# Optimization experiments

Hardware: AMD Instinct MI355X
Metric: run time of the kernel (lower is better)

## Reference

```python
import jax, jax.numpy as jnp
import numpy as np

B, N, NINP, NFEAT, H = 4096, 4096, 64, 32, 4


def setup_inputs() -> dict:
    key = jax.random.key(0)
    ks = jax.random.split(key, 8)
    s_in = 1.0 / np.sqrt(NINP)
    s_att = 1.0 / np.sqrt(2 * NFEAT)
    return {
        "X": jax.random.normal(ks[0], (B, NINP), jnp.float32),
        "G": jax.random.normal(ks[1], (N, NINP), jnp.float32),
        "A": jax.random.uniform(ks[2], (B, N), jnp.float32),  # additive mask
        "W": jax.random.uniform(ks[3], (H, NINP, NFEAT), jnp.float32, -s_in, s_in),
        "b": jax.random.uniform(ks[4], (H, NFEAT), jnp.float32, -s_in, s_in),
        "a_src": jax.random.uniform(ks[5], (H, NFEAT), jnp.float32, -s_att, s_att),
        "a_dst": jax.random.uniform(ks[6], (H, NFEAT), jnp.float32, -s_att, s_att),
        "att_b": jax.random.uniform(ks[7], (H,), jnp.float32, -s_att, s_att),
    }


def reference(X, G, A, W, b, a_src, a_dst, att_b):
    # Per-head linear transforms (all heads batched via einsum)
    WX = jnp.einsum("bi,hif->bhf", X, W) + b            # (B, H, F)
    WG = jnp.einsum("ni,hif->nhf", G, W) + b            # (N, H, F)
    # Decomposed concat-attention: a^T [WX_b ; WG_n] = a_src.WX_b + a_dst.WG_n
    s_src = jnp.einsum("bhf,hf->bh", WX, a_src)         # (B, H)
    s_dst = jnp.einsum("nhf,hf->nh", WG, a_dst)         # (N, H)
    e = s_src[:, :, None] + s_dst.T[None, :, :] + att_b[None, :, None]  # (B,H,N)
    att = jax.nn.softmax(e - A[:, None, :], axis=-1)    # adjacency-masked softmax
    # Dropout(0.5) is identity in eval mode (deterministic reference).
    out = jnp.einsum("bhn,nhf->bhf", att, WG)           # weighted aggregation
    out = jax.nn.relu(out)                              # activation before concat
    return out.reshape(out.shape[0], -1)                # (B, H*F) concat heads
```

## Files before the change

### kernel.cpp

```cpp
#include <hip/hip_runtime.h>
#include <stdint.h>

#define N_TOK 4096
#define D_IN  64
#define NF    32
#define NH    4
#define OUTW  (NH * NF)
#define NT    8
#define CHUNK 128
#define BT    32

typedef float        f32x4  __attribute__((ext_vector_type(4)));
typedef unsigned int uint4v __attribute__((ext_vector_type(4)));
typedef __bf16       bf16x8 __attribute__((ext_vector_type(8)));

union Frag { uint4v u; bf16x8 v; };

static __device__ __forceinline__ unsigned short f2bf_rne(float x) {
  unsigned u = __float_as_uint(x);
  u += 0x7fffu + ((u >> 16) & 1u);
  return (unsigned short)(u >> 16);
}

__global__ __launch_bounds__(128) void prep_kernel(
    const float* __restrict__ G, const float* __restrict__ W,
    const float* __restrict__ bias, const float* __restrict__ a_dst,
    unsigned short* __restrict__ PB) {
  __shared__ float gs[NT * D_IN];
  const int tid = threadIdx.x;
  const int n0  = blockIdx.x * NT;
  {
    const float4* src = (const float4*)(G + (size_t)n0 * D_IN);
    float4* dst = (float4*)gs;
    dst[tid] = src[tid];
  }
  __syncthreads();
  const int h = tid >> 5, f = tid & 31;
  float acc[NT];
  const float bb = bias[h * NF + f];
#pragma unroll
  for (int k = 0; k < NT; ++k) acc[k] = bb;
#pragma unroll
  for (int i = 0; i < D_IN; ++i) {
    const float wv = W[(h * D_IN + i) * NF + f];
#pragma unroll
    for (int k = 0; k < NT; ++k) acc[k] = fmaf(gs[k * D_IN + i], wv, acc[k]);
  }
  const float ad = a_dst[h * NF + f];
  float ev[NT];
#pragma unroll
  for (int k = 0; k < NT; ++k) {
    float s = acc[k] * ad;
    s += __shfl_xor(s, 1);  s += __shfl_xor(s, 2);  s += __shfl_xor(s, 4);
    s += __shfl_xor(s, 8);  s += __shfl_xor(s, 16);
    ev[k] = __expf(s);
  }
  const int t   = n0 >> 5;
  const int gq  = (n0 >> 3) & 3;
  const int set = (h << 1) | (f >> 4);
  const int col = f & 15;
  union { uint4 u4; unsigned short us[8]; } pk;
#pragma unroll
  for (int k = 0; k < NT; ++k) pk.us[k] = f2bf_rne(acc[k] * ev[k]);
  *(uint4*)(PB + (size_t)((((t * 9 + set) << 6) + (gq << 4) + col)) * 8) = pk.u4;
  if (f == 0) {
    union { uint4 u4; unsigned short us[8]; } pe;
#pragma unroll
    for (int k = 0; k < NT; ++k) pe.us[k] = f2bf_rne(ev[k]);
    *(uint4*)(PB + (size_t)((((t * 9 + 8) << 6) + (gq << 4) + h)) * 8) = pe.u4;
  }
  if (h == 0 && f >= 4 && f < 16) {
    uint4 z; z.x = 0u; z.y = 0u; z.z = 0u; z.w = 0u;
    *(uint4*)(PB + (size_t)((((t * 9 + 8) << 6) + (gq << 4) + f)) * 8) = z;
  }
}

template <int NS>
__global__ __launch_bounds__(512) void attn_kernel(
    const float* __restrict__ A, const unsigned short* __restrict__ PB,
    float* __restrict__ op, float* __restrict__ dp, float* __restrict__ out) {
  constexpr int NHALF  = N_TOK / NS;
  constexpr int NIT    = NHALF / CHUNK;
  constexpr int RINGSZ = BT * CHUNK * 2;
  __shared__ __align__(16) unsigned short ring[3 * BT * CHUNK];
  __shared__ float denLds[BT * NH];
  char* ringb = (char*)ring;

  const int tid  = threadIdx.x;
  const int lane = tid & 63;
  const int w    = tid >> 6;
  const int bid  = blockIdx.x;
  const int s    = bid & (NS - 1);
  const int b0   = (bid / NS) * BT;

  const int srow = tid >> 4, tp = tid & 15;
  const float* abase = A + (size_t)(b0 + srow) * N_TOK + s * NHALF + tp * 8;
  const int wb0 = srow * 256 + ((tp ^ (srow & 15)) << 4);

  const int rowm = lane & 15, g = lane >> 4;
  const char* pbb  = (const char*)PB + (size_t)s * (NHALF / 32) * 9216;
  const char* pown = pbb + (((w << 6) + lane) << 4);
  const char* pden = pbb + (((8 << 6) + lane) << 4);

  f32x4 acc0  = {0.f, 0.f, 0.f, 0.f}, acc1  = {0.f, 0.f, 0.f, 0.f};
  f32x4 accd0 = {0.f, 0.f, 0.f, 0.f}, accd1 = {0.f, 0.f, 0.f, 0.f};
  f32x4 aXa, aXb, aYa, aYb;
  Frag bo0, bo1, bo2, bo3, bd0, bd1, bd2, bd3;
  Frag co0, co1, co2, co3, cd0, cd1, cd2, cd3;
  int mR = 0, mW = 1;

#define LOADA2(d0, d1, cc) do {                                                \
    const float* ap_ = abase + (size_t)(cc) * CHUNK;                           \
    asm volatile("global_load_dwordx4 %0, %1, off"                            \
                 : "=v"(d0) : "v"(ap_) : "memory");                            \
    asm volatile("global_load_dwordx4 %0, %1, off"                            \
                 : "=v"(d1) : "v"(ap_ + 4) : "memory");                        \
  } while (0)
#define LOADBO(fr, cc, kk)                                                     \
  asm volatile("global_load_dwordx4 %0, %1, off"                              \
               : "=v"(fr.u)                                                    \
               : "v"(pown + (size_t)((cc) * 4 + (kk)) * 9216) : "memory")
#define LOADBD(fr, cc, kk)                                                     \
  asm volatile("global_load_dwordx4 %0, %1, off"                              \
               : "=v"(fr.u)                                                    \
               : "v"(pden + (size_t)((cc) * 4 + (kk)) * 9216) : "memory")

#define EXPP(AV0, AV1, mw) do {                                                \
    float x0 = __expf(-AV0[0]), x1 = __expf(-AV0[1]);                          \
    float x2 = __expf(-AV0[2]), x3 = __expf(-AV0[3]);                          \
    float x4 = __expf(-AV1[0]), x5 = __expf(-AV1[1]);                          \
    float x6 = __expf(-AV1[2]), x7 = __expf(-AV1[3]);                          \
    uint4v t_;                                                                 \
    t_[0] = __builtin_amdgcn_perm(__float_as_uint(x1), __float_as_uint(x0), 0x07060302u); \
    t_[1] = __builtin_amdgcn_perm(__float_as_uint(x3), __float_as_uint(x2), 0x07060302u); \
    t_[2] = __builtin_amdgcn_perm(__float_as_uint(x5), __float_as_uint(x4), 0x07060302u); \
    t_[3] = __builtin_amdgcn_perm(__float_as_uint(x7), __float_as_uint(x6), 0x07060302u); \
    *(uint4v*)(ringb + (mw) * RINGSZ + wb0) = t_;                              \
  } while (0)

#define MSTEPD(rg, kk, FB, FD) do {                                            \
    Frag af_;                                                                  \
    af_.v = *(const bf16x8*)(ringb + mR * RINGSZ + ((rg) * 16 + rowm) * 256 +  \
                             ((((kk) * 4 + g) ^ rowm) << 4));                  \
    if ((rg) == 0) {                                                           \
      acc0  = __builtin_amdgcn_mfma_f32_16x16x32_bf16(af_.v, FB.v, acc0,  0, 0, 0); \
      accd0 = __builtin_amdgcn_mfma_f32_16x16x32_bf16(af_.v, FD.v, accd0, 0, 0, 0); \
    } else {                                                                   \
      acc1  = __builtin_amdgcn_mfma_f32_16x16x32_bf16(af_.v, FB.v, acc1,  0, 0, 0); \
      accd1 = __builtin_amdgcn_mfma_f32_16x16x32_bf16(af_.v, FD.v, accd1, 0, 0, 0); \
    }                                                                          \
  } while (0)
#define MSTEPO(rg, kk, FB) do {                                                \
    Frag af_;                                                                  \
    af_.v = *(const bf16x8*)(ringb + mR * RINGSZ + ((rg) * 16 + rowm) * 256 +  \
                             ((((kk) * 4 + g) ^ rowm) << 4));                  \
    if ((rg) == 0)                                                             \
      acc0 = __builtin_amdgcn_mfma_f32_16x16x32_bf16(af_.v, FB.v, acc0, 0, 0, 0); \
    else                                                                       \
      acc1 = __builtin_amdgcn_mfma_f32_16x16x32_bf16(af_.v, FB.v, acc1, 0, 0, 0); \
  } while (0)

#define ITERD(cc, AC0, AC1, AN0, AN1, CO0, CO1, CO2, CO3, CD0, CD1, CD2, CD3,  \
              NO0, NO1, NO2, NO3, ND0, ND1, ND2, ND3) do {                     \
    { const int cb_ = ((cc) + 1 < NIT) ? (cc) + 1 : NIT - 1;                   \
      LOADBO(NO0, cb_, 0); LOADBO(NO1, cb_, 1);                                \
      LOADBO(NO2, cb_, 2); LOADBO(NO3, cb_, 3);                                \
      LOADBD(ND0, cb_, 0); LOADBD(ND1, cb_, 1);                                \
      LOADBD(ND2, cb_, 2); LOADBD(ND3, cb_, 3); }                              \
    { const int ca_ = ((cc) + 2 < NIT) ? (cc) + 2 : NIT - 1;                   \
      LOADA2(AN0, AN1, ca_); }                                                 \
    asm volatile("s_waitcnt vmcnt(10)" ::: "memory");                          \
    __builtin_amdgcn_sched_barrier(0);                                         \
    EXPP(AC0, AC1, mW);                                                        \
    asm volatile("s_waitcnt lgkmcnt(0)" ::: "memory");                         \
    __builtin_amdgcn_sched_barrier(0);                                         \
    __builtin_amdgcn_s_barrier();                                              \
    MSTEPD(0, 0, CO0, CD0); MSTEPD(1, 0, CO0, CD0);                            \
    MSTEPD(0, 1, CO1, CD1); MSTEPD(1, 1, CO1, CD1);                            \
    MSTEPD(0, 2, CO2, CD2); MSTEPD(1, 2, CO2, CD2);                            \
    MSTEPD(0, 3, CO3, CD3); MSTEPD(1, 3, CO3, CD3);                            \
    mR = mW; mW = (mW + 1 == 3) ? 0 : mW + 1;                                  \
  } while (0)
#define ITERO(cc, AC0, AC1, AN0, AN1, CO0, CO1, CO2, CO3,                      \
              NO0, NO1, NO2, NO3) do {                                         \
    { const int cb_ = ((cc) + 1 < NIT) ? (cc) + 1 : NIT - 1;                   \
      LOADBO(NO0, cb_, 0); LOADBO(NO1, cb_, 1);                                \
      LOADBO(NO2, cb_, 2); LOADBO(NO3, cb_, 3); }                              \
    { const int ca_ = ((cc) + 2 < NIT) ? (cc) + 2 : NIT - 1;                   \
      LOADA2(AN0, AN1, ca_); }                                                 \
    asm volatile("s_waitcnt vmcnt(6)" ::: "memory");                           \
    __builtin_amdgcn_sched_barrier(0);                                         \
    EXPP(AC0, AC1, mW);                                                        \
    asm volatile("s_waitcnt lgkmcnt(0)" ::: "memory");                         \
    __builtin_amdgcn_sched_barrier(0);                                         \
    __builtin_amdgcn_s_barrier();                                              \
    MSTEPO(0, 0, CO0); MSTEPO(1, 0, CO0);                                      \
    MSTEPO(0, 1, CO1); MSTEPO(1, 1, CO1);                                      \
    MSTEPO(0, 2, CO2); MSTEPO(1, 2, CO2);                                      \
    MSTEPO(0, 3, CO3); MSTEPO(1, 3, CO3);                                      \
    mR = mW; mW = (mW + 1 == 3) ? 0 : mW + 1;                                  \
  } while (0)

  if (w == 0) {
    LOADA2(aXa, aXb, 0);
    LOADBO(bo0, 0, 0); LOADBO(bo1, 0, 1); LOADBO(bo2, 0, 2); LOADBO(bo3, 0, 3);
    LOADBD(bd0, 0, 0); LOADBD(bd1, 0, 1); LOADBD(bd2, 0, 2); LOADBD(bd3, 0, 3);
    LOADA2(aYa, aYb, 1);
    asm volatile("s_waitcnt vmcnt(10)" ::: "memory");
    __builtin_amdgcn_sched_barrier(0);
    EXPP(aXa, aXb, 0);
#pragma unroll 1
    for (int i = 0; i < NIT; i += 2) {
      ITERD(i,     aYa, aYb, aXa, aXb, bo0, bo1, bo2, bo3, bd0, bd1, bd2, bd3,
                                       co0, co1, co2, co3, cd0, cd1, cd2, cd3);
      ITERD(i + 1, aXa, aXb, aYa, aYb, co0, co1, co2, co3, cd0, cd1, cd2, cd3,
                                       bo0, bo1, bo2, bo3, bd0, bd1, bd2, bd3);
    }
  } else {
    LOADA2(aXa, aXb, 0);
    LOADBO(bo0, 0, 0); LOADBO(bo1, 0, 1); LOADBO(bo2, 0, 2); LOADBO(bo3, 0, 3);
    LOADA2(aYa, aYb, 1);
    asm volatile("s_waitcnt vmcnt(6)" ::: "memory");
    __builtin_amdgcn_sched_barrier(0);
    EXPP(aXa, aXb, 0);
#pragma unroll 1
    for (int i = 0; i < NIT; i += 2) {
      ITERO(i,     aYa, aYb, aXa, aXb, bo0, bo1, bo2, bo3,
                                       co0, co1, co2, co3);
      ITERO(i + 1, aXa, aXb, aYa, aYb, co0, co1, co2, co3,
                                       bo0, bo1, bo2, bo3);
    }
  }

  asm volatile("s_waitcnt vmcnt(0)" ::: "memory");
  __builtin_amdgcn_sched_barrier(0);

  if (NS == 1) {
    if (w == 0 && rowm < NH) {
#pragma unroll
      for (int r = 0; r < 4; ++r) {
        denLds[(g * 4 + r) * NH + rowm]      = accd0[r];
        denLds[(16 + g * 4 + r) * NH + rowm] = accd1[r];
      }
    }
    __syncthreads();
    const int hh = w >> 1;
#pragma unroll
    for (int r = 0; r < 4; ++r) {
      const float o0 = acc0[r] / denLds[(g * 4 + r) * NH + hh];
      out[(size_t)(b0 + g * 4 + r) * OUTW + w * 16 + rowm] = o0 > 0.f ? o0 : 0.f;
      const float o1 = acc1[r] / denLds[(16 + g * 4 + r) * NH + hh];
      out[(size_t)(b0 + 16 + g * 4 + r) * OUTW + w * 16 + rowm] = o1 > 0.f ? o1 : 0.f;
    }
  } else {
    float* ob = op + (size_t)s * (N_TOK * OUTW) + (size_t)b0 * OUTW + w * 16 + rowm;
#pragma unroll
    for (int r = 0; r < 4; ++r) {
      ob[(size_t)(g * 4 + r) * OUTW]      = acc0[r];
      ob[(size_t)(16 + g * 4 + r) * OUTW] = acc1[r];
    }
    if (w == 0 && rowm < NH) {
#pragma unroll
      for (int r = 0; r < 4; ++r) {
        dp[((size_t)s * N_TOK + b0 + g * 4 + r) * NH + rowm]      = accd0[r];
        dp[((size_t)s * N_TOK + b0 + 16 + g * 4 + r) * NH + rowm] = accd1[r];
      }
    }
  }
#undef LOADA2
#undef LOADBO
#undef LOADBD
#undef EXPP
#undef MSTEPD
#undef MSTEPO
#undef ITERD
#undef ITERO
}

__global__ __launch_bounds__(256) void comb_kernel(
    const float* __restrict__ op, const float* __restrict__ dp,
    float* __restrict__ out, int NS) {
  const int idx4 = blockIdx.x * 256 + threadIdx.x;
  const int eb = idx4 >> 5;
  const int h  = ((idx4 << 2) & 127) >> 5;
  float4 o; o.x = 0.f; o.y = 0.f; o.z = 0.f; o.w = 0.f;
  float d = 0.f;
  for (int s2 = 0; s2 < NS; ++s2) {
    float4 vv = *(const float4*)(op + (size_t)s2 * (N_TOK * OUTW) + (size_t)idx4 * 4);
    o.x += vv.x; o.y += vv.y; o.z += vv.z; o.w += vv.w;
    d += dp[((size_t)s2 * N_TOK + eb) * NH + h];
  }
  const float r = 1.f / d;
  float4 res;
  res.x = fmaxf(o.x * r, 0.f);
  res.y = fmaxf(o.y * r, 0.f);
  res.z = fmaxf(o.z * r, 0.f);
  res.w = fmaxf(o.w * r, 0.f);
  *(float4*)(out + (size_t)idx4 * 4) = res;
}

extern "C" void kernel_launch(void* const* d_in, const int* in_sizes, int n_in,
                              void* d_out, int out_size, void* d_ws, size_t ws_size,
                              hipStream_t stream) {
  const float* G     = (const float*)d_in[1];
  const float* A     = (const float*)d_in[2];
  const float* W     = (const float*)d_in[3];
  const float* bias  = (const float*)d_in[4];
  const float* a_dst = (const float*)d_in[6];

  char* ws = (char*)d_ws;
  const size_t PBsz = (size_t)128 * 9 * 1024;
  const size_t per_split = (size_t)N_TOK * OUTW * 4 + (size_t)N_TOK * NH * 4;

  unsigned short* PB = (unsigned short*)ws;
  float* op = (float*)(ws + PBsz);
  float* outp = (float*)d_out;

  prep_kernel<<<N_TOK / NT, 128, 0, stream>>>(G, W, bias, a_dst, PB);
  if (ws_size >= PBsz + 4 * per_split) {
    float* dp = (float*)(ws + PBsz + 4 * (size_t)N_TOK * OUTW * 4);
    attn_kernel<4><<<(N_TOK / BT) * 4, 512, 0, stream>>>(A, PB, op, dp, nullptr);
    comb_kernel<<<(N_TOK * OUTW / 4) / 256, 256, 0, stream>>>(op, dp, outp, 4);
  } else if (ws_size >= PBsz + 2 * per_split) {
    float* dp = (float*)(ws + PBsz + 2 * (size_t)N_TOK * OUTW * 4);
    attn_kernel<2><<<(N_TOK / BT) * 2, 512, 0, stream>>>(A, PB, op, dp, nullptr);
    comb_kernel<<<(N_TOK * OUTW / 4) / 256, 256, 0, stream>>>(op, dp, outp, 2);
  } else {
    attn_kernel<1><<<N_TOK / BT, 512, 0, stream>>>(A, PB, nullptr, nullptr, outp);
  }
}
```

Measured before the change: 30.83 us.

## Double batch tile to 64 rows per block to reuse B fragments

Raises the batch tile per attention block from 32 to 64 rows. Each wave now keeps four accumulator groups and issues 16 MFMAs per chunk against the same loaded PB fragments, so per-row global loads of the projected G data are halved. Each thread now loads and exponentiates 16 mask values per chunk instead of 8. The cost is more register pressure, a larger LDS ring, and half as many blocks, which can hurt occupancy and how well the GPU is filled.

```diff
diff --git a/kernel.cpp b/kernel.cpp
--- a/kernel.cpp
+++ b/kernel.cpp
@@ -8,7 +8,7 @@
 #define OUTW  (NH * NF)
 #define NT    8
 #define CHUNK 128
-#define BT    32
+#define BT    64
 
 typedef float        f32x4  __attribute__((ext_vector_type(4)));
 typedef unsigned int uint4v __attribute__((ext_vector_type(4)));
@@ -93,9 +93,10 @@
   const int s    = bid & (NS - 1);
   const int b0   = (bid / NS) * BT;
 
-  const int srow = tid >> 4, tp = tid & 15;
-  const float* abase = A + (size_t)(b0 + srow) * N_TOK + s * NHALF + tp * 8;
-  const int wb0 = srow * 256 + ((tp ^ (srow & 15)) << 4);
+  const int srow = tid >> 3, tp = tid & 7;
+  const float* abase = A + (size_t)(b0 + srow) * N_TOK + s * NHALF + tp * 16;
+  const int wb0 = srow * 256 + (((tp * 2    ) ^ (srow & 15)) << 4);
+  const int wb1 = srow * 256 + (((tp * 2 + 1) ^ (srow & 15)) << 4);
 
   const int rowm = lane & 15, g = lane >> 4;
   const char* pbb  = (const char*)PB + (size_t)s * (NHALF / 32) * 9216;
@@ -103,18 +104,24 @@
   const char* pden = pbb + (((8 << 6) + lane) << 4);
 
   f32x4 acc0  = {0.f, 0.f, 0.f, 0.f}, acc1  = {0.f, 0.f, 0.f, 0.f};
+  f32x4 acc2  = {0.f, 0.f, 0.f, 0.f}, acc3  = {0.f, 0.f, 0.f, 0.f};
   f32x4 accd0 = {0.f, 0.f, 0.f, 0.f}, accd1 = {0.f, 0.f, 0.f, 0.f};
-  f32x4 aXa, aXb, aYa, aYb;
+  f32x4 accd2 = {0.f, 0.f, 0.f, 0.f}, accd3 = {0.f, 0.f, 0.f, 0.f};
+  f32x4 aXa, aXb, aXc, aXd, aYa, aYb, aYc, aYd;
   Frag bo0, bo1, bo2, bo3, bd0, bd1, bd2, bd3;
   Frag co0, co1, co2, co3, cd0, cd1, cd2, cd3;
   int mR = 0, mW = 1;
 
-#define LOADA2(d0, d1, cc) do {                                                \
+#define LOADA4(d0, d1, d2, d3, cc) do {                                        \
     const float* ap_ = abase + (size_t)(cc) * CHUNK;                           \
     asm volatile("global_load_dwordx4 %0, %1, off"                            \
                  : "=v"(d0) : "v"(ap_) : "memory");                            \
     asm volatile("global_load_dwordx4 %0, %1, off"                            \
                  : "=v"(d1) : "v"(ap_ + 4) : "memory");                        \
+    asm volatile("global_load_dwordx4 %0, %1, off"                            \
+                 : "=v"(d2) : "v"(ap_ + 8) : "memory");                        \
+    asm volatile("global_load_dwordx4 %0, %1, off"                            \
+                 : "=v"(d3) : "v"(ap_ + 12) : "memory");                       \
   } while (0)
 #define LOADBO(fr, cc, kk)                                                     \
   asm volatile("global_load_dwordx4 %0, %1, off"                              \
@@ -125,42 +132,44 @@
                : "=v"(fr.u)                                                    \
                : "v"(pden + (size_t)((cc) * 4 + (kk)) * 9216) : "memory")
 
-#define EXPP(AV0, AV1, mw) do {                                                \
+#define EXPP(AV0, AV1, AV2, AV3, mw) do {                                      \
     float x0 = __expf(-AV0[0]), x1 = __expf(-AV0[1]);                          \
     float x2 = __expf(-AV0[2]), x3 = __expf(-AV0[3]);                          \
     float x4 = __expf(-AV1[0]), x5 = __expf(-AV1[1]);                          \
     float x6 = __expf(-AV1[2]), x7 = __expf(-AV1[3]);                          \
-    uint4v t_;                                                                 \
+    float y0 = __expf(-AV2[0]), y1 = __expf(-AV2[1]);                          \
+    float y2 = __expf(-AV2[2]), y3 = __expf(-AV2[3]);                          \
+    float y4 = __expf(-AV3[0]), y5 = __expf(-AV3[1]);                          \
+    float y6 = __expf(-AV3[2]), y7 = __expf(-AV3[3]);                          \
+    uint4v t_, u_;                                                             \
     t_[0] = __builtin_amdgcn_perm(__float_as_uint(x1), __float_as_uint(x0), 0x07060302u); \
     t_[1] = __builtin_amdgcn_perm(__float_as_uint(x3), __float_as_uint(x2), 0x07060302u); \
     t_[2] = __builtin_amdgcn_perm(__float_as_uint(x5), __float_as_uint(x4), 0x07060302u); \
     t_[3] = __builtin_amdgcn_perm(__float_as_uint(x7), __float_as_uint(x6), 0x07060302u); \
-    *(uint4v*)(ringb + (mw) * RINGSZ + wb0) = t_;                              \
-  } while (0)
-
-#define MSTEPD(rg, kk, FB, FD) do {                                            \
-    Frag af_;                                                                  \
-    af_.v = *(const bf16x8*)(ringb + mR * RINGSZ + ((rg) * 16 + rowm) * 256 +  \
-                             ((((kk) * 4 + g) ^ rowm) << 4));                  \
-    if ((rg) == 0) {                                                           \
-      acc0  = __builtin_amdgcn_mfma_f32_16x16x32_bf16(af_.v, FB.v, acc0,  0, 0, 0); \
-      accd0 = __builtin_amdgcn_mfma_f32_16x16x32_bf16(af_.v, FD.v, accd0, 0, 0, 0); \
-    } else {                                                                   \
-      acc1  = __builtin_amdgcn_mfma_f32_16x16x32_bf16(af_.v, FB.v, acc1,  0, 0, 0); \
-      accd1 = __builtin_amdgcn_mfma_f32_16x16x32_bf16(af_.v, FD.v, accd1, 0, 0, 0); \
-    }                                                                          \
-  } while (0)
-#define MSTEPO(rg, kk, FB) do {                                                \
-    Frag af_;                                                                  \
-    af_.v = *(const bf16x8*)(ringb + mR * RINGSZ + ((rg) * 16 + rowm) * 256 +  \
-                             ((((kk) * 4 + g) ^ rowm) << 4));                  \
-    if ((rg) == 0)                                                             \
-      acc0 = __builtin_amdgcn_mfma_f32_16x16x32_bf16(af_.v, FB.v, acc0, 0, 0, 0); \
-    else                                                                       \
-      acc1 = __builtin_amdgcn_mfma_f32_16x16x32_bf16(af_.v, FB.v, acc1, 0, 0, 0); \
-  } while (0)
-
-#define ITERD(cc, AC0, AC1, AN0, AN1, CO0, CO1, CO2, CO3, CD0, CD1, CD2, CD3,  \
+    u_[0] = __builtin_amdgcn_perm(__float_as_uint(y1), __float_as_uint(y0), 0x07060302u); \
+    u_[1] = __builtin_amdgcn_perm(__float_as_uint(y3), __float_as_uint(y2), 0x07060302u); \
+    u_[2] = __builtin_amdgcn_perm(__float_as_uint(y5), __float_as_uint(y4), 0x07060302u); \
+    u_[3] = __builtin_amdgcn_perm(__float_as_uint(y7), __float_as_uint(y6), 0x07060302u); \
+    char* rb_ = ringb + (mw) * RINGSZ;                                         \
+    *(uint4v*)(rb_ + wb0) = t_;                                                \
+    *(uint4v*)(rb_ + wb1) = u_;                                                \
+  } while (0)
+
+#define AF(rg, kk)                                                             \
+  (*(const bf16x8*)(ringb + mR * RINGSZ + ((rg) * 16 + rowm) * 256 +           \
+                    ((((kk) * 4 + g) ^ rowm) << 4)))
+#define MQD(ACC, ACCD, rg, kk, FB, FD) do {                                    \
+    Frag af_; af_.v = AF(rg, kk);                                              \
+    ACC  = __builtin_amdgcn_mfma_f32_16x16x32_bf16(af_.v, FB.v, ACC,  0, 0, 0);\
+    ACCD = __builtin_amdgcn_mfma_f32_16x16x32_bf16(af_.v, FD.v, ACCD, 0, 0, 0);\
+  } while (0)
+#define MQO(ACC, rg, kk, FB) do {                                              \
+    Frag af_; af_.v = AF(rg, kk);                                              \
+    ACC = __builtin_amdgcn_mfma_f32_16x16x32_bf16(af_.v, FB.v, ACC, 0, 0, 0);  \
+  } while (0)
+
+#define ITERD(cc, AC0, AC1, AC2, AC3, AN0, AN1, AN2, AN3,                      \
+              CO0, CO1, CO2, CO3, CD0, CD1, CD2, CD3,                          \
               NO0, NO1, NO2, NO3, ND0, ND1, ND2, ND3) do {                     \
     { const int cb_ = ((cc) + 1 < NIT) ? (cc) + 1 : NIT - 1;                   \
       LOADBO(NO0, cb_, 0); LOADBO(NO1, cb_, 1);                                \
@@ -168,67 +177,77 @@
       LOADBD(ND0, cb_, 0); LOADBD(ND1, cb_, 1);                                \
       LOADBD(ND2, cb_, 2); LOADBD(ND3, cb_, 3); }                              \
     { const int ca_ = ((cc) + 2 < NIT) ? (cc) + 2 : NIT - 1;                   \
-      LOADA2(AN0, AN1, ca_); }                                                 \
-    asm volatile("s_waitcnt vmcnt(10)" ::: "memory");                          \
+      LOADA4(AN0, AN1, AN2, AN3, ca_); }                                       \
+    asm volatile("s_waitcnt vmcnt(12)" ::: "memory");                          \
     __builtin_amdgcn_sched_barrier(0);                                         \
-    EXPP(AC0, AC1, mW);                                                        \
+    EXPP(AC0, AC1, AC2, AC3, mW);                                              \
     asm volatile("s_waitcnt lgkmcnt(0)" ::: "memory");                         \
     __builtin_amdgcn_sched_barrier(0);                                         \
     __builtin_amdgcn_s_barrier();                                              \
-    MSTEPD(0, 0, CO0, CD0); MSTEPD(1, 0, CO0, CD0);                            \
-    MSTEPD(0, 1, CO1, CD1); MSTEPD(1, 1, CO1, CD1);                            \
-    MSTEPD(0, 2, CO2, CD2); MSTEPD(1, 2, CO2, CD2);                            \
-    MSTEPD(0, 3, CO3, CD3); MSTEPD(1, 3, CO3, CD3);                            \
+    MQD(acc0, accd0, 0, 0, CO0, CD0); MQD(acc1, accd1, 1, 0, CO0, CD0);        \
+    MQD(acc2, accd2, 2, 0, CO0, CD0); MQD(acc3, accd3, 3, 0, CO0, CD0);        \
+    MQD(acc0, accd0, 0, 1, CO1, CD1); MQD(acc1, accd1, 1, 1, CO1, CD1);        \
+    MQD(acc2, accd2, 2, 1, CO1, CD1); MQD(acc3, accd3, 3, 1, CO1, CD1);        \
+    MQD(acc0, accd0, 0, 2, CO2, CD2); MQD(acc1, accd1, 1, 2, CO2, CD2);        \
+    MQD(acc2, accd2, 2, 2, CO2, CD2); MQD(acc3, accd3, 3, 2, CO2, CD2);        \
+    MQD(acc0, accd0, 0, 3, CO3, CD3); MQD(acc1, accd1, 1, 3, CO3, CD3);        \
+    MQD(acc2, accd2, 2, 3, CO3, CD3); MQD(acc3, accd3, 3, 3, CO3, CD3);        \
     mR = mW; mW = (mW + 1 == 3) ? 0 : mW + 1;                                  \
   } while (0)
-#define ITERO(cc, AC0, AC1, AN0, AN1, CO0, CO1, CO2, CO3,                      \
-              NO0, NO1, NO2, NO3) do {                                         \
+#define ITERO(cc, AC0, AC1, AC2, AC3, AN0, AN1, AN2, AN3,                      \
+              CO0, CO1, CO2, CO3, NO0, NO1, NO2, NO3) do {                     \
     { const int cb_ = ((cc) + 1 < NIT) ? (cc) + 1 : NIT - 1;                   \
       LOADBO(NO0, cb_, 0); LOADBO(NO1, cb_, 1);                                \
       LOADBO(NO2, cb_, 2); LOADBO(NO3, cb_, 3); }                              \
     { const int ca_ = ((cc) + 2 < NIT) ? (cc) + 2 : NIT - 1;                   \
-      LOADA2(AN0, AN1, ca_); }                                                 \
-    asm volatile("s_waitcnt vmcnt(6)" ::: "memory");                           \
+      LOADA4(AN0, AN1, AN2, AN3, ca_); }                                       \
+    asm volatile("s_waitcnt vmcnt(8)" ::: "memory");                           \
     __builtin_amdgcn_sched_barrier(0);                                         \
-    EXPP(AC0, AC1, mW);                                                        \
+    EXPP(AC0, AC1, AC2, AC3, mW);                                              \
     asm volatile("s_waitcnt lgkmcnt(0)" ::: "memory");                         \
     __builtin_amdgcn_sched_barrier(0);                                         \
     __builtin_amdgcn_s_barrier();                                              \
-    MSTEPO(0, 0, CO0); MSTEPO(1, 0, CO0);                                      \
-    MSTEPO(0, 1, CO1); MSTEPO(1, 1, CO1);                                      \
-    MSTEPO(0, 2, CO2); MSTEPO(1, 2, CO2);                                      \
-    MSTEPO(0, 3, CO3); MSTEPO(1, 3, CO3);                                      \
+    MQO(acc0, 0, 0, CO0); MQO(acc1, 1, 0, CO0);                                \
+    MQO(acc2, 2, 0, CO0); MQO(acc3, 3, 0, CO0);                                \
+    MQO(acc0, 0, 1, CO1); MQO(acc1, 1, 1, CO1);                                \
+    MQO(acc2, 2, 1, CO1); MQO(acc3, 3, 1, CO1);                                \
+    MQO(acc0, 0, 2, CO2); MQO(acc1, 1, 2, CO2);                                \
+    MQO(acc2, 2, 2, CO2); MQO(acc3, 3, 2, CO2);                                \
+    MQO(acc0, 0, 3, CO3); MQO(acc1, 1, 3, CO3);                                \
+    MQO(acc2, 2, 3, CO3); MQO(acc3, 3, 3, CO3);                                \
     mR = mW; mW = (mW + 1 == 3) ? 0 : mW + 1;                                  \
   } while (0)
 
   if (w == 0) {
-    LOADA2(aXa, aXb, 0);
+    LOADA4(aXa, aXb, aXc, aXd, 0);
     LOADBO(bo0, 0, 0); LOADBO(bo1, 0, 1); LOADBO(bo2, 0, 2); LOADBO(bo3, 0, 3);
     LOADBD(bd0, 0, 0); LOADBD(bd1, 0, 1); LOADBD(bd2, 0, 2); LOADBD(bd3, 0, 3);
-    LOADA2(aYa, aYb, 1);
-    asm volatile("s_waitcnt vmcnt(10)" ::: "memory");
+    LOADA4(aYa, aYb, aYc, aYd, 1);
+    asm volatile("s_waitcnt vmcnt(12)" ::: "memory");
     __builtin_amdgcn_sched_barrier(0);
-    EXPP(aXa, aXb, 0);
+    EXPP(aXa, aXb, aXc, aXd, 0);
 #pragma unroll 1
     for (int i = 0; i < NIT; i += 2) {
-      ITERD(i,     aYa, aYb, aXa, aXb, bo0, bo1, bo2, bo3, bd0, bd1, bd2, bd3,
-                                       co0, co1, co2, co3, cd0, cd1, cd2, cd3);
-      ITERD(i + 1, aXa, aXb, aYa, aYb, co0, co1, co2, co3, cd0, cd1, cd2, cd3,
-                                       bo0, bo1, bo2, bo3, bd0, bd1, bd2, bd3);
+      ITERD(i,     aYa, aYb, aYc, aYd, aXa, aXb, aXc, aXd,
+                   bo0, bo1, bo2, bo3, bd0, bd1, bd2, bd3,
+                   co0, co1, co2, co3, cd0, cd1, cd2, cd3);
+      ITERD(i + 1, aXa, aXb, aXc, aXd, aYa, aYb, aYc, aYd,
+                   co0, co1, co2, co3, cd0, cd1, cd2, cd3,
+                   bo0, bo1, bo2, bo3, bd0, bd1, bd2, bd3);
     }
   } else {
-    LOADA2(aXa, aXb, 0);
+    LOADA4(aXa, aXb, aXc, aXd, 0);
     LOADBO(bo0, 0, 0); LOADBO(bo1, 0, 1); LOADBO(bo2, 0, 2); LOADBO(bo3, 0, 3);
-    LOADA2(aYa, aYb, 1);
-    asm volatile("s_waitcnt vmcnt(6)" ::: "memory");
+    LOADA4(aYa, aYb, aYc, aYd, 1);
+    asm volatile("s_waitcnt vmcnt(8)" ::: "memory");
     __builtin_amdgcn_sched_barrier(0);
-    EXPP(aXa, aXb, 0);
+    EXPP(aXa, aXb, aXc, aXd, 0);
 #pragma unroll 1
     for (int i = 0; i < NIT; i += 2) {
-      ITERO(i,     aYa, aYb, aXa, aXb, bo0, bo1, bo2, bo3,
-                                       co0, co1, co2, co3);
-      ITERO(i + 1, aXa, aXb, aYa, aYb, co0, co1, co2, co3,
-                                       bo0, bo1, bo2, bo3);
+      ITERO(i,     aYa, aYb, aYc, aYd, aXa, aXb, aXc, aXd,
+                   bo0, bo1, bo2, bo3, co0, co1, co2, co3);
+      ITERO(i + 1, aXa, aXb, aXc, aXd, aYa, aYb, aYc, aYd,
+                   co0, co1, co2, co3, bo0, bo1, bo2, bo3);
     }
   }
 
@@ -239,40 +258,55 @@
     if (w == 0 && rowm < NH) {
 #pragma unroll
       for (int r = 0; r < 4; ++r) {
-        denLds[(g * 4 + r) * NH + rowm]      = accd0[r];
+        denLds[(     g * 4 + r) * NH + rowm] = accd0[r];
         denLds[(16 + g * 4 + r) * NH + rowm] = accd1[r];
+        denLds[(32 + g * 4 + r) * NH + rowm] = accd2[r];
+        denLds[(48 + g * 4 + r) * NH + rowm] = accd3[r];
       }
     }
     __syncthreads();
     const int hh = w >> 1;
 #pragma unroll
     for (int r = 0; r < 4; ++r) {
-      const float o0 = acc0[r] / denLds[(g * 4 + r) * NH + hh];
-      out[(size_t)(b0 + g * 4 + r) * OUTW + w * 16 + rowm] = o0 > 0.f ? o0 : 0.f;
-      const float o1 = acc1[r] / denLds[(16 + g * 4 + r) * NH + hh];
-      out[(size_t)(b0 + 16 + g * 4 + r) * OUTW + w * 16 + rowm] = o1 > 0.f ? o1 : 0.f;
+      const int rr = g * 4 + r;
+      float o;
+      o = acc0[r] / denLds[(     rr) * NH + hh];
+      out[(size_t)(b0 +      rr) * OUTW + w * 16 + rowm] = o > 0.f ? o : 0.f;
+      o = acc1[r] / denLds[(16 + rr) * NH + hh];
+      out[(size_t)(b0 + 16 + rr) * OUTW + w * 16 + rowm] = o > 0.f ? o : 0.f;
+      o = acc2[r] / denLds[(32 + rr) * NH + hh];
+      out[(size_t)(b0 + 32 + rr) * OUTW + w * 16 + rowm] = o > 0.f ? o : 0.f;
+      o = acc3[r] / denLds[(48 + rr) * NH + hh];
+      out[(size_t)(b0 + 48 + rr) * OUTW + w * 16 + rowm] = o > 0.f ? o : 0.f;
     }
   } else {
     float* ob = op + (size_t)s * (N_TOK * OUTW) + (size_t)b0 * OUTW + w * 16 + rowm;
 #pragma unroll
     for (int r = 0; r < 4; ++r) {
-      ob[(size_t)(g * 4 + r) * OUTW]      = acc0[r];
-      ob[(size_t)(16 + g * 4 + r) * OUTW] = acc1[r];
+      const int rr = g * 4 + r;
+      ob[(size_t)(     rr) * OUTW] = acc0[r];
+      ob[(size_t)(16 + rr) * OUTW] = acc1[r];
+      ob[(size_t)(32 + rr) * OUTW] = acc2[r];
+      ob[(size_t)(48 + rr) * OUTW] = acc3[r];
     }
     if (w == 0 && rowm < NH) {
 #pragma unroll
       for (int r = 0; r < 4; ++r) {
-        dp[((size_t)s * N_TOK + b0 + g * 4 + r) * NH + rowm]      = accd0[r];
-        dp[((size_t)s * N_TOK + b0 + 16 + g * 4 + r) * NH + rowm] = accd1[r];
+        const int rr = g * 4 + r;
+        dp[((size_t)s * N_TOK + b0 +      rr) * NH + rowm] = accd0[r];
+        dp[((size_t)s * N_TOK + b0 + 16 + rr) * NH + rowm] = accd1[r];
+        dp[((size_t)s * N_TOK + b0 + 32 + rr) * NH + rowm] = accd2[r];
+        dp[((size_t)s * N_TOK + b0 + 48 + rr) * NH + rowm] = accd3[r];
       }
     }
   }
-#undef LOADA2
+#undef LOADA4
 #undef LOADBO
 #undef LOADBD
 #undef EXPP
-#undef MSTEPD
-#undef MSTEPO
+#undef AF
+#undef MQD
+#undef MQO
 #undef ITERD
 #undef ITERO
 }
```

After: 32.49 us. 1.05x slower.
